# Kernel optimization log

Measured on AMD Instinct MI355X. Metric: run time of the kernel, lower is better.

## Reference

```python
import jax, jax.numpy as jnp
import numpy as np

DIM = 384
DEPTH = 4
HEADS = 6
DIM_HEAD = 64
INNER = HEADS * DIM_HEAD  # 384
MLP = 1536
B, N = 4, 2048


def setup_inputs() -> dict:
    key = jax.random.key(0)
    ks = jax.random.split(key, 7)
    s = 0.02
    x = jax.random.normal(ks[0], (B, N, DIM), dtype=jnp.float32)
    Wqkv = jax.random.normal(ks[1], (DEPTH, DIM, 3 * INNER), dtype=jnp.float32) * s
    Wout = jax.random.normal(ks[2], (DEPTH, INNER, DIM), dtype=jnp.float32) * s
    W1 = jax.random.normal(ks[3], (DEPTH, DIM, MLP), dtype=jnp.float32) * s
    b1 = jax.random.normal(ks[4], (DEPTH, MLP), dtype=jnp.float32) * s
    W2 = jax.random.normal(ks[5], (DEPTH, MLP, DIM), dtype=jnp.float32) * s
    b2 = jax.random.normal(ks[6], (DEPTH, DIM), dtype=jnp.float32) * s
    return {"x": x, "Wqkv": Wqkv, "Wout": Wout, "W1": W1, "b1": b1, "W2": W2, "b2": b2}


def _attention(x, Wqkv_l, Wout_l):
    scale = DIM_HEAD ** (-0.5)
    qkv = jnp.einsum('bnd,de->bne', x, Wqkv_l)  # [B,N,3*INNER]
    q, k, v = jnp.split(qkv, 3, axis=-1)
    # [B,N,INNER] -> [B,H,N,Dh]
    reshape = lambda t: t.reshape(B, N, HEADS, DIM_HEAD).transpose(0, 2, 1, 3)
    q, k, v = reshape(q), reshape(k), reshape(v)
    dots = jnp.einsum('bhnd,bhmd->bhnm', q, k) * scale
    attn = jax.nn.softmax(dots, axis=-1)
    out = jnp.einsum('bhnm,bhmd->bhnd', attn, v)
    out = out.transpose(0, 2, 1, 3).reshape(B, N, INNER)
    return jnp.einsum('bne,ed->bnd', out, Wout_l)


def _ff(x, W1_l, b1_l, W2_l, b2_l):
    h = jax.nn.gelu(jnp.einsum('bnd,dh->bnh', x, W1_l) + b1_l, approximate=False)
    return jnp.einsum('bnh,hd->bnd', h, W2_l) + b2_l


def reference(x, Wqkv, Wout, W1, b1, W2, b2):
    for l in range(DEPTH):
        x = _attention(x, Wqkv[l], Wout[l]) + x
        x = _ff(x, W1[l], b1[l], W2[l], b2[l]) + x
    return x
```

## Files before the change

kernel.cpp:

```cpp
#include <hip/hip_runtime.h>
#include <stdint.h>

#define HEADS 6
#define NN 2048
#define BB 4
#define MTOT (BB*NN)
#define DEPTH 4

typedef unsigned short u16;
typedef __attribute__((ext_vector_type(8))) short bf16x8;
typedef __attribute__((ext_vector_type(4))) float f32x4;
typedef __attribute__((ext_vector_type(16))) float f32x16;

#define MFMA32(a,b,c) __builtin_amdgcn_mfma_f32_32x32x16_bf16((a),(b),(c),0,0,0)

#define QSC 0.18033688011112042f

__device__ __forceinline__ u16 f2bf(float f) {
  union { float f; uint32_t u; } v; v.f = f;
  uint32_t r = v.u + 0x7fffu + ((v.u >> 16) & 1u);
  return (u16)(r >> 16);
}

__device__ __forceinline__ uint32_t pk2(float lo, float hi) {
  uint32_t r;
  asm("v_cvt_pk_bf16_f32 %0, %1, %2" : "=v"(r) : "v"(lo), "v"(hi));
  return r;
}

__device__ __forceinline__ void gload_lds16(const void* g, void* l) {
  __builtin_amdgcn_global_load_lds((const __attribute__((address_space(1))) void*)g,
                                   (__attribute__((address_space(3))) void*)l, 16, 0, 0);
}

__global__ __launch_bounds__(256)
void wtrans_k(const float* __restrict__ in, u16* __restrict__ out, int K, int N) {
  __shared__ float t[32][33];
  const int z = blockIdx.z;
  in  += (size_t)z * K * N;
  out += (size_t)z * K * N;
  const int n0 = blockIdx.x * 32, k0 = blockIdx.y * 32;
  const int tx = threadIdx.x & 31, ty = threadIdx.x >> 5;
#pragma unroll
  for (int i = 0; i < 4; ++i)
    t[ty + i*8][tx] = in[(size_t)(k0 + ty + i*8) * N + n0 + tx];
  __syncthreads();
#pragma unroll
  for (int i = 0; i < 4; ++i)
    out[(size_t)(n0 + ty + i*8) * K + k0 + tx] = f2bf(t[tx][ty + i*8]);
}

__global__ __launch_bounds__(256)
void xprep_k(const float* __restrict__ x, u16* __restrict__ xbf, int n) {
  int i = blockIdx.x * 256 + threadIdx.x;
  if (i < n) xbf[i] = f2bf(x[i]);
}

template<int MODE>
__global__ __launch_bounds__(256)
void gemm64_k(const u16* __restrict__ A, const u16* __restrict__ Bt,
              const float* __restrict__ bias, const float* __restrict__ res,
              float* __restrict__ outF, u16* __restrict__ outB,
              u16* __restrict__ qb, u16* __restrict__ kb, u16* __restrict__ vtb,
              int M, int N, int K) {
  __shared__ u16 smA[64 * 64];
  __shared__ u16 smB[64 * 64];
  const int tid = threadIdx.x;
  const int lane = tid & 63, wv = tid >> 6;
  const int wr = wv >> 1, wc = wv & 1;
  const int l31 = lane & 31, h2 = lane >> 5;
  const int row0 = blockIdx.y * 64, col0 = blockIdx.x * 64;

  f32x16 acc;
#pragma unroll
  for (int i = 0; i < 16; ++i) acc[i] = 0.f;

  const int c0 = tid, c1 = tid + 256;
  const int r0 = c0 >> 3, s0 = (c0 & 7) ^ (r0 & 7);
  const int r1 = c1 >> 3, s1 = (c1 & 7) ^ (r1 & 7);

  const int ksteps = K >> 6;
  for (int kt = 0; kt < ksteps; ++kt) {
    const int k0 = kt << 6;
    const u16* Ab = A  + (size_t)row0 * K + k0;
    const u16* Bb = Bt + (size_t)col0 * K + k0;
    gload_lds16(Ab + (size_t)r0 * K + s0 * 8, smA + wv * 512);
    gload_lds16(Ab + (size_t)r1 * K + s1 * 8, smA + 2048 + wv * 512);
    gload_lds16(Bb + (size_t)r0 * K + s0 * 8, smB + wv * 512);
    gload_lds16(Bb + (size_t)r1 * K + s1 * 8, smB + 2048 + wv * 512);
    __syncthreads();
    const int ra = wr * 32 + l31;
    const int rb = wc * 32 + l31;
#pragma unroll
    for (int ks = 0; ks < 4; ++ks) {
      bf16x8 af = *(const bf16x8*)(smA + ra * 64 + (((ks * 2 + h2) ^ (ra & 7)) * 8));
      bf16x8 bf = *(const bf16x8*)(smB + rb * 64 + (((ks * 2 + h2) ^ (rb & 7)) * 8));
      acc = MFMA32(af, bf, acc);
    }
    __syncthreads();
  }

  const int col = col0 + wc * 32 + l31;
#pragma unroll
  for (int c = 0; c < 4; ++c)
#pragma unroll
    for (int j = 0; j < 4; ++j) {
      const int row = row0 + wr * 32 + 8 * c + 4 * h2 + j;
      float v = acc[4 * c + j];
      if (MODE == 1) {
        size_t idx = (size_t)row * N + col;
        v += res[idx];
        outF[idx] = v;
        outB[idx] = f2bf(v);
      } else if (MODE == 2) {
        v += bias[col];
        v = 0.5f * v * (1.0f + erff(v * 0.70710678118f));
        outB[(size_t)row * N + col] = f2bf(v);
      } else {
        size_t idx = (size_t)row * N + col;
        v += bias[col] + res[idx];
        outF[idx] = v;
        outB[idx] = f2bf(v);
      }
    }
}

template<int MODE>
__global__ __launch_bounds__(256)
void gemmA_k(const u16* __restrict__ A, const u16* __restrict__ Bt,
             const float* __restrict__ bias,
             u16* __restrict__ outB,
             u16* __restrict__ qb, u16* __restrict__ kb, u16* __restrict__ vtb,
             int M, int N, int K) {
  __shared__ u16 smA[128 * 64];
  __shared__ u16 smB[64 * 64];
  const int tid = threadIdx.x;
  const int lane = tid & 63, wv = tid >> 6;
  const int l31 = lane & 31, h2 = lane >> 5;
  const int row0 = blockIdx.y * 128, col0 = blockIdx.x * 64;

  f32x16 acc[2];
#pragma unroll
  for (int ni = 0; ni < 2; ++ni)
#pragma unroll
    for (int i = 0; i < 16; ++i) acc[ni][i] = 0.f;

  int rA[4], sA[4];
#pragma unroll
  for (int t = 0; t < 4; ++t) {
    const int c = t * 256 + tid;
    rA[t] = c >> 3; sA[t] = (c & 7) ^ (rA[t] & 7);
  }
  int rB[2], sB[2];
#pragma unroll
  for (int t = 0; t < 2; ++t) {
    const int c = t * 256 + tid;
    rB[t] = c >> 3; sB[t] = (c & 7) ^ (rB[t] & 7);
  }

  const int ksteps = K >> 6;
  const int ra = wv * 32 + l31;
  for (int kt = 0; kt < ksteps; ++kt) {
    const int k0 = kt << 6;
    const u16* Ab = A  + (size_t)row0 * K + k0;
    const u16* Bb = Bt + (size_t)col0 * K + k0;
#pragma unroll
    for (int t = 0; t < 4; ++t)
      gload_lds16(Ab + (size_t)rA[t] * K + sA[t] * 8, smA + t * 2048 + wv * 512);
#pragma unroll
    for (int t = 0; t < 2; ++t)
      gload_lds16(Bb + (size_t)rB[t] * K + sB[t] * 8, smB + t * 2048 + wv * 512);
    __syncthreads();
#pragma unroll
    for (int ks = 0; ks < 4; ++ks) {
      bf16x8 af = *(const bf16x8*)(smA + ra * 64 + (((ks * 2 + h2) ^ (ra & 7)) * 8));
#pragma unroll
      for (int ni = 0; ni < 2; ++ni) {
        const int rb = ni * 32 + l31;
        bf16x8 bf = *(const bf16x8*)(smB + rb * 64 + (((ks * 2 + h2) ^ (rb & 7)) * 8));
        acc[ni] = MFMA32(af, bf, acc[ni]);
      }
    }
    __syncthreads();
  }

  if (MODE == 0) {
#pragma unroll
    for (int ni = 0; ni < 2; ++ni) {
      const int col = col0 + ni * 32 + l31;
      const int sec = col / 384, c3 = col - sec * 384;
      const int hh = c3 >> 6, d = c3 & 63;
#pragma unroll
      for (int c = 0; c < 4; ++c)
#pragma unroll
        for (int j = 0; j < 4; ++j) {
          const int row = row0 + wv * 32 + 8 * c + 4 * h2 + j;
          const int bb = row >> 11, n = row & 2047;
          const float v = acc[ni][4 * c + j];
          if (sec == 0)       qb [(((size_t)bb * HEADS + hh) * NN + n) * 64 + d] = f2bf(v * QSC);
          else if (sec == 1)  kb [(((size_t)bb * HEADS + hh) * NN + n) * 64 + d] = f2bf(v);
          else                vtb[(((size_t)bb * HEADS + hh) * 64 + d) * NN + n] = f2bf(v);
        }
    }
  } else {
#pragma unroll
    for (int ni = 0; ni < 2; ++ni) {
      const int col = col0 + ni * 32 + l31;
#pragma unroll
      for (int c = 0; c < 4; ++c)
#pragma unroll
        for (int j = 0; j < 4; ++j) {
          const int row = row0 + wv * 32 + 8 * c + 4 * h2 + j;
          float v = acc[ni][4 * c + j] + bias[col];
          v = 0.5f * v * (1.0f + erff(v * 0.70710678118f));
          outB[(size_t)row * N + col] = f2bf(v);
        }
    }
  }
}

__global__ __launch_bounds__(256)
void attn_k(const u16* __restrict__ qb, const u16* __restrict__ kb,
            const u16* __restrict__ vtb, u16* __restrict__ ob) {
  __shared__ u16 kb3[3][2][32 * 64];
  __shared__ u16 vb3[3][2][64 * 32];
  const int tid = threadIdx.x;
  const int lane = tid & 63, wv = tid >> 6;
  const int l31 = lane & 31, h2 = lane >> 5;
  const int hs = wv >> 1;
  const int qg = wv & 1;

  const int lid = blockIdx.y * 32 + blockIdx.x;
  const int xcd = lid & 7, ii = lid >> 3;
  const int bh = 3 * xcd + (ii >> 5);
  const int qblk = ii & 31;
  const int b = bh / HEADS, h = bh - b * HEADS;
  const int q0 = qblk * 64 + qg * 32;

  const u16* Qb = qb + ((size_t)bh * NN + q0 + l31) * 64;
  bf16x8 qf[4];
#pragma unroll
  for (int ct2 = 0; ct2 < 4; ++ct2)
    qf[ct2] = *(const bf16x8*)(Qb + ct2 * 16 + h2 * 8);

  float m = -1e30f, s = 0.f;
  f32x16 acc[2];
#pragma unroll
  for (int dg = 0; dg < 2; ++dg)
#pragma unroll
    for (int i = 0; i < 16; ++i) acc[dg][i] = 0.f;
  const f32x16 zero16 = {0.f,0.f,0.f,0.f,0.f,0.f,0.f,0.f,0.f,0.f,0.f,0.f,0.f,0.f,0.f,0.f};

  const u16* Kb0 = kb  + (size_t)bh * NN * 64;
  const u16* Vt0 = vtb + (size_t)bh * 64 * NN;
  const int rK = tid >> 3, sK = (tid & 7) ^ (rK & 7);
  const int rV = tid >> 2, sV = (tid & 3) ^ (rV & 3);

#define STAGE3(kd, vd, t) do { \
    _Pragma("unroll") \
    for (int hf = 0; hf < 2; ++hf) { \
      gload_lds16(Kb0 + ((size_t)(hf * 1024 + (t) * 32 + rK)) * 64 + sK * 8, \
                  (kd) + hf * 2048 + wv * 512); \
      gload_lds16(Vt0 + (size_t)rV * NN + hf * 1024 + (t) * 32 + sV * 8, \
                  (vd) + hf * 2048 + wv * 512); \
    } \
  } while (0)

  u16 *kA = &kb3[0][0][0], *kB = &kb3[1][0][0], *kC = &kb3[2][0][0];
  u16 *vA = &vb3[0][0][0], *vB = &vb3[1][0][0], *vC = &vb3[2][0][0];

  STAGE3(kA, vA, 0);
  __syncthreads();

  bf16x8 pf[2];
  const int NT = 1024 / 32;
  for (int kt = 0; kt < NT; ++kt) {
    if (kt + 1 < NT) STAGE3(kB, vB, kt + 1);

    f32x16 st = zero16;
    {
      const u16* krow = kA + hs * 2048 + l31 * 64;
#pragma unroll
      for (int ct2 = 0; ct2 < 4; ++ct2) {
        bf16x8 kf = *(const bf16x8*)(krow + (((ct2 * 2 + h2) ^ (l31 & 7)) * 8));
        st = MFMA32(kf, qf[ct2], st);
      }
    }
    if (kt > 0) {
#pragma unroll
      for (int ks = 0; ks < 2; ++ks)
#pragma unroll
        for (int dg = 0; dg < 2; ++dg) {
          const int d = dg * 32 + l31;
          bf16x8 vf = *(const bf16x8*)(vC + hs * 2048 + d * 32 + (((ks * 2 + h2) ^ (d & 3)) * 8));
          acc[dg] = MFMA32(vf, pf[ks], acc[dg]);
        }
    }

    float tmax = -1e30f;
#pragma unroll
    for (int i = 0; i < 16; ++i) tmax = fmaxf(tmax, st[i]);
    if (!__all(tmax <= m + 8.0f)) {
      float rm = fmaxf(tmax, __shfl_xor(tmax, 32));
      float mn = fmaxf(m, rm);
      float al = __builtin_amdgcn_exp2f(m - mn);
      s *= al;
#pragma unroll
      for (int dg = 0; dg < 2; ++dg)
#pragma unroll
        for (int i = 0; i < 16; ++i) acc[dg][i] *= al;
      m = mn;
    }
    float p[16];
    float r = 0.f;
#pragma unroll
    for (int i = 0; i < 16; ++i) {
      float t = __builtin_amdgcn_exp2f(st[i] - m);
      p[i] = t;
      r += t;
    }
    r += __shfl_xor(r, 32);
    s += r;

#pragma unroll
    for (int sub = 0; sub < 2; ++sub) {
      const int s8 = sub * 8;
      uint32_t X0 = pk2(p[s8 + 0], p[s8 + 1]);
      uint32_t X1 = pk2(p[s8 + 2], p[s8 + 3]);
      uint32_t Y0 = pk2(p[s8 + 4], p[s8 + 5]);
      uint32_t Y1 = pk2(p[s8 + 6], p[s8 + 7]);
      asm volatile("v_permlane32_swap_b32 %0, %1" : "+v"(X0), "+v"(Y0));
      asm volatile("v_permlane32_swap_b32 %0, %1" : "+v"(X1), "+v"(Y1));
      union { uint32_t u[4]; bf16x8 v; } pu;
      pu.u[0] = X0; pu.u[1] = X1; pu.u[2] = Y0; pu.u[3] = Y1;
      pf[sub] = pu.v;
    }

    __syncthreads();
    u16* t1 = kA; kA = kB; kB = kC; kC = t1;
    u16* t2 = vA; vA = vB; vB = vC; vC = t2;
  }

#pragma unroll
  for (int ks = 0; ks < 2; ++ks)
#pragma unroll
    for (int dg = 0; dg < 2; ++dg) {
      const int d = dg * 32 + l31;
      bf16x8 vf = *(const bf16x8*)(vC + hs * 2048 + d * 32 + (((ks * 2 + h2) ^ (d & 3)) * 8));
      acc[dg] = MFMA32(vf, pf[ks], acc[dg]);
    }

  float* mb = (float*)kb3;
  if (wv >= 2) {
    const int base = ((wv - 2) * 64 + lane) * 36;
#pragma unroll
    for (int dg = 0; dg < 2; ++dg)
#pragma unroll
      for (int i = 0; i < 16; ++i) mb[base + dg * 16 + i] = acc[dg][i];
    mb[base + 32] = m;
    mb[base + 33] = s;
  }
  __syncthreads();
  if (wv < 2) {
    const int base = (wv * 64 + lane) * 36;
    const float m2 = mb[base + 32], s2 = mb[base + 33];
    const float M  = fmaxf(m, m2);
    const float a1 = __builtin_amdgcn_exp2f(m  - M);
    const float a2 = __builtin_amdgcn_exp2f(m2 - M);
    const float inv = 1.f / (s * a1 + s2 * a2);
    u16* orow = ob + ((size_t)b * NN + q0 + l31) * 384 + h * 64;
#pragma unroll
    for (int dg = 0; dg < 2; ++dg)
#pragma unroll
      for (int c = 0; c < 4; ++c) {
        float v0 = (acc[dg][4*c + 0] * a1 + mb[base + dg*16 + 4*c + 0] * a2) * inv;
        float v1 = (acc[dg][4*c + 1] * a1 + mb[base + dg*16 + 4*c + 1] * a2) * inv;
        float v2 = (acc[dg][4*c + 2] * a1 + mb[base + dg*16 + 4*c + 2] * a2) * inv;
        float v3 = (acc[dg][4*c + 3] * a1 + mb[base + dg*16 + 4*c + 3] * a2) * inv;
        uint2 w;
        w.x = pk2(v0, v1);
        w.y = pk2(v2, v3);
        *(uint2*)(orow + dg * 32 + 8 * c + 4 * h2) = w;
      }
  }
}

extern "C" void kernel_launch(void* const* d_in, const int* in_sizes, int n_in,
                              void* d_out, int out_size, void* d_ws, size_t ws_size,
                              hipStream_t stream) {
  (void)in_sizes; (void)n_in; (void)out_size; (void)ws_size;
  const float* x    = (const float*)d_in[0];
  const float* Wqkv = (const float*)d_in[1];
  const float* Wout = (const float*)d_in[2];
  const float* W1   = (const float*)d_in[3];
  const float* b1   = (const float*)d_in[4];
  const float* W2   = (const float*)d_in[5];
  const float* b2   = (const float*)d_in[6];
  float* out = (float*)d_out;

  char* ws = (char*)d_ws;
  size_t off = 0;
  auto alloc = [&](size_t bytes) { char* p = ws + off; off += (bytes + 255) & ~(size_t)255; return p; };
  u16*   wqkvT = (u16*)alloc((size_t)DEPTH * 1152 * 384 * 2);
  u16*   woutT = (u16*)alloc((size_t)DEPTH * 384 * 384 * 2);
  u16*   w1T   = (u16*)alloc((size_t)DEPTH * 1536 * 384 * 2);
  u16*   w2T   = (u16*)alloc((size_t)DEPTH * 384 * 1536 * 2);
  u16*   xbf   = (u16*)alloc((size_t)MTOT * 384 * 2);
  float* xres  = (float*)alloc((size_t)MTOT * 384 * 4);
  u16*   qbuf  = (u16*)alloc((size_t)MTOT * 384 * 2);
  u16*   kbuf  = (u16*)alloc((size_t)MTOT * 384 * 2);
  u16*   vtbuf = (u16*)alloc((size_t)MTOT * 384 * 2);
  u16*   obuf  = (u16*)alloc((size_t)MTOT * 384 * 2);
  u16*   hbuf  = (u16*)alloc((size_t)MTOT * 1536 * 2);

  wtrans_k<<<dim3(1152/32, 384/32, DEPTH), 256, 0, stream>>>(Wqkv, wqkvT, 384, 1152);
  wtrans_k<<<dim3( 384/32, 384/32, DEPTH), 256, 0, stream>>>(Wout, woutT, 384, 384);
  wtrans_k<<<dim3(1536/32, 384/32, DEPTH), 256, 0, stream>>>(W1,   w1T,   384, 1536);
  wtrans_k<<<dim3( 384/32,1536/32, DEPTH), 256, 0, stream>>>(W2,   w2T,   1536, 384);
  xprep_k<<<(MTOT*384 + 255)/256, 256, 0, stream>>>(x, xbf, MTOT*384);

  for (int l = 0; l < DEPTH; ++l) {
    gemmA_k<0><<<dim3(1152/64, MTOT/128), 256, 0, stream>>>(
        xbf, wqkvT + (size_t)l*1152*384, nullptr, nullptr,
        qbuf, kbuf, vtbuf, MTOT, 1152, 384);
    attn_k<<<dim3(32, 24), 256, 0, stream>>>(qbuf, kbuf, vtbuf, obuf);
    gemm64_k<1><<<dim3(384/64, MTOT/64), 256, 0, stream>>>(
        obuf, woutT + (size_t)l*384*384, nullptr, (l == 0 ? x : xres), xres, xbf,
        nullptr, nullptr, nullptr, MTOT, 384, 384);
    gemmA_k<2><<<dim3(1536/64, MTOT/128), 256, 0, stream>>>(
        xbf, w1T + (size_t)l*1536*384, b1 + l*1536, hbuf,
        nullptr, nullptr, nullptr, MTOT, 1536, 384);
    gemm64_k<3><<<dim3(384/64, MTOT/64), 256, 0, stream>>>(
        hbuf, w2T + (size_t)l*384*1536, b2 + l*384, xres,
        (l == DEPTH-1 ? out : xres), xbf,
        nullptr, nullptr, nullptr, MTOT, 384, 1536);
  }
}
```

Measured before the change: 551.4 us.

## Use 128x128 tiles with 512 threads for QKV and FF1 GEMMs, XCD-aware block remap

Replaces the 128x64-tile, 256-thread GEMM used for the QKV projection and the first FF layer with a 128x128-tile, 512-thread kernel. Each wave now computes a 64x32 sub-tile, so every loaded B fragment is reused across two MFMAs and less global traffic is spent per output. It also remaps block IDs so that contiguous tile ranges land on the same XCD, for L2 locality, in both GEMM kernels. The cost is fewer blocks (e.g. 576 for QKV), which may underfill the 256 CUs, and larger LDS use per block.

```diff
diff --git a/kernel.cpp b/kernel.cpp
--- a/kernel.cpp
+++ b/kernel.cpp
@@ -69,7 +69,12 @@
   const int lane = tid & 63, wv = tid >> 6;
   const int wr = wv >> 1, wc = wv & 1;
   const int l31 = lane & 31, h2 = lane >> 5;
-  const int row0 = blockIdx.y * 64, col0 = blockIdx.x * 64;
+
+  const int gx = gridDim.x;
+  const int lid = blockIdx.y * gx + blockIdx.x;
+  const int chunk = (gx * gridDim.y) >> 3;
+  const int v_ = (lid & 7) * chunk + (lid >> 3);
+  const int row0 = (v_ / gx) * 64, col0 = (v_ % gx) * 64;
 
   f32x16 acc;
 #pragma unroll
@@ -101,121 +106,129 @@
   }
 
   const int col = col0 + wc * 32 + l31;
-#pragma unroll
-  for (int c = 0; c < 4; ++c)
-#pragma unroll
-    for (int j = 0; j < 4; ++j) {
-      const int row = row0 + wr * 32 + 8 * c + 4 * h2 + j;
-      float v = acc[4 * c + j];
-      if (MODE == 1) {
-        size_t idx = (size_t)row * N + col;
-        v += res[idx];
-        outF[idx] = v;
-        outB[idx] = f2bf(v);
-      } else if (MODE == 2) {
-        v += bias[col];
-        v = 0.5f * v * (1.0f + erff(v * 0.70710678118f));
-        outB[(size_t)row * N + col] = f2bf(v);
-      } else {
-        size_t idx = (size_t)row * N + col;
-        v += bias[col] + res[idx];
-        outF[idx] = v;
-        outB[idx] = f2bf(v);
+  if (MODE == 0) {
+    const int sec = col / 384, c3 = col - sec * 384;
+    const int hh = c3 >> 6, d = c3 & 63;
+#pragma unroll
+    for (int c = 0; c < 4; ++c)
+#pragma unroll
+      for (int j = 0; j < 4; ++j) {
+        const int row = row0 + wr * 32 + 8 * c + 4 * h2 + j;
+        const int bb = row >> 11, n = row & 2047;
+        const float v = acc[4 * c + j];
+        if (sec == 0)       qb [(((size_t)bb * HEADS + hh) * NN + n) * 64 + d] = f2bf(v * QSC);
+        else if (sec == 1)  kb [(((size_t)bb * HEADS + hh) * NN + n) * 64 + d] = f2bf(v);
+        else                vtb[(((size_t)bb * HEADS + hh) * 64 + d) * NN + n] = f2bf(v);
       }
-    }
+  } else {
+#pragma unroll
+    for (int c = 0; c < 4; ++c)
+#pragma unroll
+      for (int j = 0; j < 4; ++j) {
+        const int row = row0 + wr * 32 + 8 * c + 4 * h2 + j;
+        float v = acc[4 * c + j];
+        if (MODE == 1) {
+          size_t idx = (size_t)row * N + col;
+          v += res[idx];
+          outF[idx] = v;
+          outB[idx] = f2bf(v);
+        } else if (MODE == 2) {
+          v += bias[col];
+          v = 0.5f * v * (1.0f + erff(v * 0.70710678118f));
+          outB[(size_t)row * N + col] = f2bf(v);
+        } else {
+          size_t idx = (size_t)row * N + col;
+          v += bias[col] + res[idx];
+          outF[idx] = v;
+          outB[idx] = f2bf(v);
+        }
+      }
+  }
 }
 
 template<int MODE>
-__global__ __launch_bounds__(256)
-void gemmA_k(const u16* __restrict__ A, const u16* __restrict__ Bt,
-             const float* __restrict__ bias,
-             u16* __restrict__ outB,
-             u16* __restrict__ qb, u16* __restrict__ kb, u16* __restrict__ vtb,
-             int M, int N, int K) {
+__global__ __launch_bounds__(512)
+void gemm128_k(const u16* __restrict__ A, const u16* __restrict__ Bt,
+               const float* __restrict__ bias,
+               u16* __restrict__ outB,
+               u16* __restrict__ qb, u16* __restrict__ kb, u16* __restrict__ vtb,
+               int M, int N, int K) {
   __shared__ u16 smA[128 * 64];
-  __shared__ u16 smB[64 * 64];
+  __shared__ u16 smB[128 * 64];
   const int tid = threadIdx.x;
   const int lane = tid & 63, wv = tid >> 6;
+  const int wr = wv >> 2, wc = wv & 3;
   const int l31 = lane & 31, h2 = lane >> 5;
-  const int row0 = blockIdx.y * 128, col0 = blockIdx.x * 64;
+
+  const int gx = gridDim.x;
+  const int lid = blockIdx.y * gx + blockIdx.x;
+  const int chunk = (gx * gridDim.y) >> 3;
+  const int v_ = (lid & 7) * chunk + (lid >> 3);
+  const int row0 = (v_ / gx) * 128, col0 = (v_ % gx) * 128;
 
   f32x16 acc[2];
 #pragma unroll
-  for (int ni = 0; ni < 2; ++ni)
-#pragma unroll
-    for (int i = 0; i < 16; ++i) acc[ni][i] = 0.f;
-
-  int rA[4], sA[4];
-#pragma unroll
-  for (int t = 0; t < 4; ++t) {
-    const int c = t * 256 + tid;
-    rA[t] = c >> 3; sA[t] = (c & 7) ^ (rA[t] & 7);
-  }
-  int rB[2], sB[2];
-#pragma unroll
-  for (int t = 0; t < 2; ++t) {
-    const int c = t * 256 + tid;
-    rB[t] = c >> 3; sB[t] = (c & 7) ^ (rB[t] & 7);
-  }
+  for (int mi = 0; mi < 2; ++mi)
+#pragma unroll
+    for (int i = 0; i < 16; ++i) acc[mi][i] = 0.f;
+
+  const int c0 = tid, c1 = tid + 512;
+  const int r0 = c0 >> 3, s0 = (c0 & 7) ^ (r0 & 7);
+  const int r1 = c1 >> 3, s1 = (c1 & 7) ^ (r1 & 7);
 
   const int ksteps = K >> 6;
-  const int ra = wv * 32 + l31;
   for (int kt = 0; kt < ksteps; ++kt) {
     const int k0 = kt << 6;
     const u16* Ab = A  + (size_t)row0 * K + k0;
     const u16* Bb = Bt + (size_t)col0 * K + k0;
-#pragma unroll
-    for (int t = 0; t < 4; ++t)
-      gload_lds16(Ab + (size_t)rA[t] * K + sA[t] * 8, smA + t * 2048 + wv * 512);
-#pragma unroll
-    for (int t = 0; t < 2; ++t)
-      gload_lds16(Bb + (size_t)rB[t] * K + sB[t] * 8, smB + t * 2048 + wv * 512);
+    gload_lds16(Ab + (size_t)r0 * K + s0 * 8, smA + tid * 8);
+    gload_lds16(Ab + (size_t)r1 * K + s1 * 8, smA + 4096 + tid * 8);
+    gload_lds16(Bb + (size_t)r0 * K + s0 * 8, smB + tid * 8);
+    gload_lds16(Bb + (size_t)r1 * K + s1 * 8, smB + 4096 + tid * 8);
     __syncthreads();
+    const int rb = wc * 32 + l31;
 #pragma unroll
     for (int ks = 0; ks < 4; ++ks) {
-      bf16x8 af = *(const bf16x8*)(smA + ra * 64 + (((ks * 2 + h2) ^ (ra & 7)) * 8));
-#pragma unroll
-      for (int ni = 0; ni < 2; ++ni) {
-        const int rb = ni * 32 + l31;
-        bf16x8 bf = *(const bf16x8*)(smB + rb * 64 + (((ks * 2 + h2) ^ (rb & 7)) * 8));
-        acc[ni] = MFMA32(af, bf, acc[ni]);
+      bf16x8 bf = *(const bf16x8*)(smB + rb * 64 + (((ks * 2 + h2) ^ (rb & 7)) * 8));
+#pragma unroll
+      for (int mi = 0; mi < 2; ++mi) {
+        const int ra = wr * 64 + mi * 32 + l31;
+        bf16x8 af = *(const bf16x8*)(smA + ra * 64 + (((ks * 2 + h2) ^ (ra & 7)) * 8));
+        acc[mi] = MFMA32(af, bf, acc[mi]);
       }
     }
     __syncthreads();
   }
 
+  const int col = col0 + wc * 32 + l31;
   if (MODE == 0) {
-#pragma unroll
-    for (int ni = 0; ni < 2; ++ni) {
-      const int col = col0 + ni * 32 + l31;
-      const int sec = col / 384, c3 = col - sec * 384;
-      const int hh = c3 >> 6, d = c3 & 63;
+    const int sec = col / 384, c3 = col - sec * 384;
+    const int hh = c3 >> 6, d = c3 & 63;
+#pragma unroll
+    for (int mi = 0; mi < 2; ++mi)
 #pragma unroll
       for (int c = 0; c < 4; ++c)
 #pragma unroll
         for (int j = 0; j < 4; ++j) {
-          const int row = row0 + wv * 32 + 8 * c + 4 * h2 + j;
+          const int row = row0 + wr * 64 + mi * 32 + 8 * c + 4 * h2 + j;
           const int bb = row >> 11, n = row & 2047;
-          const float v = acc[ni][4 * c + j];
+          const float v = acc[mi][4 * c + j];
           if (sec == 0)       qb [(((size_t)bb * HEADS + hh) * NN + n) * 64 + d] = f2bf(v * QSC);
           else if (sec == 1)  kb [(((size_t)bb * HEADS + hh) * NN + n) * 64 + d] = f2bf(v);
           else                vtb[(((size_t)bb * HEADS + hh) * 64 + d) * NN + n] = f2bf(v);
         }
-    }
   } else {
 #pragma unroll
-    for (int ni = 0; ni < 2; ++ni) {
-      const int col = col0 + ni * 32 + l31;
+    for (int mi = 0; mi < 2; ++mi)
 #pragma unroll
       for (int c = 0; c < 4; ++c)
 #pragma unroll
         for (int j = 0; j < 4; ++j) {
-          const int row = row0 + wv * 32 + 8 * c + 4 * h2 + j;
-          float v = acc[ni][4 * c + j] + bias[col];
+          const int row = row0 + wr * 64 + mi * 32 + 8 * c + 4 * h2 + j;
+          float v = acc[mi][4 * c + j] + bias[col];
           v = 0.5f * v * (1.0f + erff(v * 0.70710678118f));
           outB[(size_t)row * N + col] = f2bf(v);
         }
-    }
   }
 }
 
@@ -420,14 +433,14 @@
   xprep_k<<<(MTOT*384 + 255)/256, 256, 0, stream>>>(x, xbf, MTOT*384);
 
   for (int l = 0; l < DEPTH; ++l) {
-    gemmA_k<0><<<dim3(1152/64, MTOT/128), 256, 0, stream>>>(
+    gemm128_k<0><<<dim3(1152/128, MTOT/128), 512, 0, stream>>>(
         xbf, wqkvT + (size_t)l*1152*384, nullptr, nullptr,
         qbuf, kbuf, vtbuf, MTOT, 1152, 384);
     attn_k<<<dim3(32, 24), 256, 0, stream>>>(qbuf, kbuf, vtbuf, obuf);
     gemm64_k<1><<<dim3(384/64, MTOT/64), 256, 0, stream>>>(
         obuf, woutT + (size_t)l*384*384, nullptr, (l == 0 ? x : xres), xres, xbf,
         nullptr, nullptr, nullptr, MTOT, 384, 384);
-    gemmA_k<2><<<dim3(1536/64, MTOT/128), 256, 0, stream>>>(
+    gemm128_k<2><<<dim3(1536/128, MTOT/128), 512, 0, stream>>>(
         xbf, w1T + (size_t)l*1536*384, b1 + l*1536, hbuf,
         nullptr, nullptr, nullptr, MTOT, 1536, 384);
     gemm64_k<3><<<dim3(384/64, MTOT/64), 256, 0, stream>>>(
```

After: 510.7 us. 7.4% less time.
